# Kernel tuning notes

Hardware: AMD Instinct MI355X
Metric: run time of the kernel (lower is better)

The kernel has to match this reference:

```python
import jax, jax.numpy as jnp
import numpy as np

TEMP = 0.07  # softmax temperature T


def _l2norm(x, axis=1, eps=1e-12):
    return x / jnp.clip(jnp.linalg.norm(x, axis=axis, keepdims=True), eps, None)


def setup_inputs() -> dict:
    key = jax.random.key(0)
    k1, k2, k3, k4 = jax.random.split(key, 4)
    B, K, D = 256, 8192, 128
    q = jax.random.normal(k1, (B, D), dtype=jnp.float32)
    ba_queue = _l2norm(jax.random.normal(k2, (K, D), dtype=jnp.float32))
    nonba_queue = _l2norm(jax.random.normal(k3, (K, D), dtype=jnp.float32))
    targets = jax.random.randint(k4, (B,), 0, 2, dtype=jnp.int64)
    return {"q": q, "ba_queue": ba_queue, "nonba_queue": nonba_queue, "targets": targets}


def reference(q, ba_queue, nonba_queue, targets):
    K = ba_queue.shape[0]
    # encoder output is L2-normalized; queues are detached buffers
    qn = _l2norm(q, axis=1)
    all_feature = jnp.concatenate([qn, ba_queue, nonba_queue], axis=0)  # [N, D]
    all_label = jnp.concatenate([
        targets.astype(jnp.int32),
        jnp.ones((K,), dtype=jnp.int32),
        jnp.zeros((K,), dtype=jnp.int32),
    ])  # [N]
    N = all_feature.shape[0]

    # [N, N] similarity logits
    sim = jnp.matmul(all_feature, all_feature.T) / TEMP
    logits = sim - jax.lax.stop_gradient(jnp.max(sim, axis=1, keepdims=True))

    # positive mask (same label), excluding self
    mask = (all_label[:, None] == all_label[None, :]).astype(jnp.float32)
    logits_mask = 1.0 - jnp.eye(N, dtype=jnp.float32)
    mask = mask * logits_mask

    exp_logits = jnp.exp(logits) * logits_mask
    log_prob = logits - jnp.log(jnp.sum(exp_logits, axis=1, keepdims=True))
    mean_log_prob_pos = jnp.sum(mask * log_prob, axis=1) / jnp.sum(mask, axis=1)
    return -jnp.mean(mean_log_prob_pos)
```

## Files before the change

### kernel.cpp

```cpp
#include <hip/hip_runtime.h>
#include <hip/hip_bf16.h>
#include <stdint.h>

#define TEMPERATURE 0.07f
#define SC 20.6099312f

constexpr int NQ = 256;
constexpr int KQ = 8192;
constexpr int D  = 128;
constexpr int N  = NQ + 2 * KQ;
constexpr int CS = 26;
constexpr int BN = 128;
constexpr int RBM = N / 128;
constexpr int RBF = N / 256;

typedef float f32x16 __attribute__((ext_vector_type(16)));
typedef int   i32x4  __attribute__((ext_vector_type(4)));
typedef int   i32x8  __attribute__((ext_vector_type(8)));

constexpr size_t OFF_F32  = 0;
constexpr size_t OFF_8    = OFF_F32  + (size_t)NQ * D * 4;
constexpr size_t OFF_8S   = OFF_8    + (size_t)N * D;
constexpr size_t OFF_PART = OFF_8S   + (size_t)N * D;
constexpr size_t OFF_LP   = OFF_PART + (size_t)CS * N * 4;
constexpr size_t OFF_BSUM = OFF_LP   + (size_t)260 * 2 * 128 * 4;

#define MFMA8(a, b, c) __builtin_amdgcn_mfma_scale_f32_32x32x64_f8f6f4( \
    (a), (b), (c), 0, 0, 0, 0x7f7f7f7f, 0, 0x7f7f7f7f)

__global__ __launch_bounds__(256) void k_prep(const float* __restrict__ q,
                                              const float* __restrict__ ba,
                                              const float* __restrict__ nb,
                                              const long long* __restrict__ tgt,
                                              float* __restrict__ ff,
                                              unsigned char* __restrict__ fb8,
                                              unsigned char* __restrict__ fb8s,
                                              float* __restrict__ lp) {
    __shared__ float red[4][2][128];
    int wid = threadIdx.x >> 6, lane = threadIdx.x & 63;
    int rbase = blockIdx.x * 64 + wid * 16;
    float s0x = 0.f, s0y = 0.f, s1x = 0.f, s1y = 0.f;
    for (int i = 0; i < 16; ++i) {
        int r = rbase + i;
        const float* src = (r < NQ) ? (q + (size_t)r * D)
                         : (r < NQ + KQ) ? (ba + (size_t)(r - NQ) * D)
                         : (nb + (size_t)(r - NQ - KQ) * D);
        float2 v = *(const float2*)(src + lane * 2);
        float a = v.x, b = v.y;
        int lab;
        if (r < NQ) {
            float ss = a * a + b * b;
            #pragma unroll
            for (int m = 1; m < 64; m <<= 1) ss += __shfl_xor(ss, m);
            float scale = 1.0f / fmaxf(sqrtf(ss), 1e-12f);
            a *= scale; b *= scale;
            lab = (int)tgt[r];
            *(float2*)(ff + (size_t)r * D + lane * 2) = make_float2(a, b);
        } else {
            lab = (r < NQ + KQ) ? 1 : 0;
        }
        int w8  = __builtin_amdgcn_cvt_pk_fp8_f32(a, b, 0, false);
        int w8s = __builtin_amdgcn_cvt_pk_fp8_f32(a * SC, b * SC, 0, false);
        *(unsigned short*)(fb8  + (size_t)r * D + lane * 2) = (unsigned short)w8;
        *(unsigned short*)(fb8s + (size_t)r * D + lane * 2) = (unsigned short)w8s;
        if (lab) { s1x += a; s1y += b; } else { s0x += a; s0y += b; }
    }
    red[wid][0][lane * 2]     = s0x;
    red[wid][0][lane * 2 + 1] = s0y;
    red[wid][1][lane * 2]     = s1x;
    red[wid][1][lane * 2 + 1] = s1y;
    __syncthreads();
    int lab2 = threadIdx.x >> 7, d = threadIdx.x & 127;
    float s = red[0][lab2][d] + red[1][lab2][d] + red[2][lab2][d] + red[3][lab2][d];
    lp[((size_t)blockIdx.x * 2 + lab2) * 128 + d] = s;
}

__device__ __forceinline__ i32x8 lda(const unsigned char* buf, int wc, int l31,
                                     int lhi, int s, int cc) {
    int crow = wc * 64 + cc * 32 + l31;
    int line = crow >> 1;
    int pb = ((crow & 1) << 3) + s * 4 + lhi * 2;
    const unsigned char* lb = buf + line * 256;
    i32x4 lo = *(const i32x4*)(lb + ((pb    ) ^ (line & 15)) * 16);
    i32x4 hi = *(const i32x4*)(lb + ((pb + 1) ^ (line & 15)) * 16);
    i32x8 a = {lo[0], lo[1], lo[2], lo[3], hi[0], hi[1], hi[2], hi[3]};
    return a;
}

#define FIN(c) if (dofin) { const f32x16& A = pacc[((c) >> 2) & 1][((c) >> 1) & 1]; \
    float s_ = 0.f; \
    _Pragma("unroll") \
    for (int e = 0; e < 8; ++e) s_ += __builtin_amdgcn_exp2f(A[(((c) & 1) << 3) + e]); \
    ps[((c) >> 1) & 1] += s_; }

__device__ __forceinline__ void phase(const unsigned char* buf,
                                      f32x16 (&acc)[2][2], const f32x16 (&pacc)[2][2],
                                      const i32x8 (&rf)[2][2], const f32x16& z16,
                                      int wc, int l31, int lhi, bool dofin,
                                      float (&rsum)[2]) {
    i32x8 a00 = lda(buf, wc, l31, lhi, 0, 0);
    i32x8 a10 = lda(buf, wc, l31, lhi, 1, 0);
    i32x8 a01 = lda(buf, wc, l31, lhi, 0, 1);
    i32x8 a11 = lda(buf, wc, l31, lhi, 1, 1);
    float ps[2] = {0.f, 0.f};
    acc[0][0] = MFMA8(a00, rf[0][0], z16);       FIN(0)
    acc[0][0] = MFMA8(a10, rf[0][1], acc[0][0]); FIN(1)
    acc[0][1] = MFMA8(a00, rf[1][0], z16);       FIN(2)
    acc[0][1] = MFMA8(a10, rf[1][1], acc[0][1]); FIN(3)
    acc[1][0] = MFMA8(a01, rf[0][0], z16);       FIN(4)
    acc[1][0] = MFMA8(a11, rf[0][1], acc[1][0]); FIN(5)
    acc[1][1] = MFMA8(a01, rf[1][0], z16);       FIN(6)
    acc[1][1] = MFMA8(a11, rf[1][1], acc[1][1]); FIN(7)
    if (dofin) { rsum[0] += ps[0]; rsum[1] += ps[1]; }
}

__device__ __forceinline__ void fin_all(const f32x16 (&pacc)[2][2], float (&rsum)[2]) {
    #pragma unroll
    for (int cc = 0; cc < 2; ++cc)
        #pragma unroll
        for (int rs = 0; rs < 2; ++rs) {
            float p = 0.f;
            #pragma unroll
            for (int g = 0; g < 16; ++g)
                p += __builtin_amdgcn_exp2f(pacc[cc][rs][g]);
            rsum[rs] += p;
        }
}

__global__ __launch_bounds__(256, 2) void k_main(const unsigned char* __restrict__ fb8,
                                                 const unsigned char* __restrict__ fb8s,
                                                 float* __restrict__ part) {
    __shared__ __align__(16) unsigned char lds[2][BN * 128];
    const int bid = blockIdx.x;
    const int rb = bid / CS, cs = bid % CS;
    const int tid = threadIdx.x;
    const int lane = tid & 63;
    const int wid  = tid >> 6;
    const int wr = wid >> 1, wc = wid & 1;
    const int l31 = lane & 31, lhi = lane >> 5;
    const int rw = rb * 128 + wr * 64;

    int soff[4];
    #pragma unroll
    for (int i = 0; i < 4; ++i) {
        int flat = i * 256 + tid;
        int line = flat >> 4, p = flat & 15;
        int pl = p ^ (line & 15);
        soff[i] = (2 * line + (pl >> 3)) * 128 + (pl & 7) * 16;
    }

#define STAGE(T, B) { \
    const unsigned char* base_ = fb8 + ((size_t)(cs + (T) * CS)) * (BN * 128); \
    _Pragma("unroll") \
    for (int i_ = 0; i_ < 4; ++i_) \
        __builtin_amdgcn_global_load_lds( \
            (const __attribute__((address_space(1))) unsigned int*)(base_ + soff[i_]), \
            (__attribute__((address_space(3))) unsigned int*)(&lds[B][(i_ * 256 + tid) * 16]), \
            16, 0, 0); }

#define SYNC() { asm volatile("s_waitcnt vmcnt(0)" ::: "memory"); __builtin_amdgcn_s_barrier(); }

    i32x8 rf[2][2];
    #pragma unroll
    for (int rs = 0; rs < 2; ++rs)
        #pragma unroll
        for (int s = 0; s < 2; ++s)
            rf[rs][s] = *(const i32x8*)(fb8s + (size_t)(rw + rs * 32 + l31) * D + s * 64 + lhi * 32);

    f32x16 z16;
    #pragma unroll
    for (int e = 0; e < 16; ++e) z16[e] = 0.f;

    float rsum[2] = {0.f, 0.f};
    f32x16 accA[2][2], accB[2][2];

    STAGE(0, 0) SYNC()
    STAGE(1, 1)
    phase(lds[0], accA, accB, rf, z16, wc, l31, lhi, false, rsum);
    SYNC()
    STAGE(2, 0)
    phase(lds[1], accB, accA, rf, z16, wc, l31, lhi, true, rsum);
    SYNC()
    STAGE(3, 1)
    phase(lds[0], accA, accB, rf, z16, wc, l31, lhi, true, rsum);
    SYNC()
    STAGE(4, 0)
    phase(lds[1], accB, accA, rf, z16, wc, l31, lhi, true, rsum);
    SYNC()
    phase(lds[0], accA, accB, rf, z16, wc, l31, lhi, true, rsum);
    fin_all(accA, rsum);

    rsum[0] += __shfl_xor(rsum[0], 32);
    rsum[1] += __shfl_xor(rsum[1], 32);
    __shared__ float xred[2][2][32];
    if (wc == 0 && lane < 32) {
        xred[wr][0][lane] = rsum[0];
        xred[wr][1][lane] = rsum[1];
    }
    __syncthreads();
    if (wc == 1 && lane < 32) {
        part[(size_t)cs * N + rw + lane]      = xred[wr][0][lane] + rsum[0];
        part[(size_t)cs * N + rw + 32 + lane] = xred[wr][1][lane] + rsum[1];
    }
#undef STAGE
#undef SYNC
}

__global__ __launch_bounds__(256) void k_rowfin(const float* __restrict__ part,
                                                const float* __restrict__ ff,
                                                const float* __restrict__ ba,
                                                const float* __restrict__ nb,
                                                const float* __restrict__ lp,
                                                const long long* __restrict__ tgt,
                                                float* __restrict__ bsum) {
    __shared__ float sS[256];
    __shared__ float red[256];
    __shared__ int scnt[2];
    {
        int lab = threadIdx.x >> 7, d = threadIdx.x & 127;
        float s[4] = {0.f, 0.f, 0.f, 0.f};
        for (int b = 0; b < 260; b += 4) {
            #pragma unroll
            for (int j = 0; j < 4; ++j)
                s[j] += lp[((size_t)(b + j) * 2 + lab) * 128 + d];
        }
        sS[threadIdx.x] = (s[0] + s[1]) + (s[2] + s[3]);
        if (threadIdx.x < 64) {
            int c = 0;
            #pragma unroll
            for (int i = 0; i < 4; ++i) c += (int)tgt[threadIdx.x + 64 * i];
            #pragma unroll
            for (int m = 1; m < 64; m <<= 1) c += __shfl_xor(c, m);
            if (threadIdx.x == 0) { scnt[0] = (NQ - c) + KQ; scnt[1] = c + KQ; }
        }
    }
    __syncthreads();
    int r = blockIdx.x * 256 + threadIdx.x;
    float se = 0.f;
    #pragma unroll
    for (int c = 0; c < CS; ++c) se += part[(size_t)c * N + r];
    int lab = (r < NQ) ? (int)tgt[r] : ((r < NQ + KQ) ? 1 : 0);
    const float* fsrc = (r < NQ) ? (ff + (size_t)r * D)
                      : (r < NQ + KQ) ? (ba + (size_t)(r - NQ) * D)
                      : (nb + (size_t)(r - NQ - KQ) * D);
    const float4* frow = (const float4*)fsrc;
    const float4* srow = (const float4*)(sS + lab * 128);
    float dS = 0.f, dd = 0.f;
    #pragma unroll
    for (int i = 0; i < 32; ++i) {
        float4 f = frow[i];
        float4 s = srow[i];
        dS += f.x * s.x + f.y * s.y + f.z * s.z + f.w * s.w;
        int wa  = __builtin_amdgcn_cvt_pk_fp8_f32(f.x, f.y, 0, false);
        int wb  = __builtin_amdgcn_cvt_pk_fp8_f32(f.z, f.w, 0, false);
        int wsa = __builtin_amdgcn_cvt_pk_fp8_f32(f.x * SC, f.y * SC, 0, false);
        int wsb = __builtin_amdgcn_cvt_pk_fp8_f32(f.z * SC, f.w * SC, 0, false);
        dd += __builtin_amdgcn_cvt_f32_fp8(wa, 0) * __builtin_amdgcn_cvt_f32_fp8(wsa, 0)
            + __builtin_amdgcn_cvt_f32_fp8(wa, 1) * __builtin_amdgcn_cvt_f32_fp8(wsa, 1)
            + __builtin_amdgcn_cvt_f32_fp8(wb, 0) * __builtin_amdgcn_cvt_f32_fp8(wsb, 0)
            + __builtin_amdgcn_cvt_f32_fp8(wb, 1) * __builtin_amdgcn_cvt_f32_fp8(wsb, 1);
    }
    se -= __builtin_amdgcn_exp2f(dd);
    float lse = logf(se);
    float P = (float)(scnt[lab] - 1);
    float mlpp = (dS - 1.0f) / (TEMPERATURE * P) - lse;
    red[threadIdx.x] = mlpp;
    __syncthreads();
    for (int s2 = 128; s2 > 0; s2 >>= 1) {
        if (threadIdx.x < s2) red[threadIdx.x] += red[threadIdx.x + s2];
        __syncthreads();
    }
    if (threadIdx.x == 0) bsum[blockIdx.x] = red[0];
}

__global__ __launch_bounds__(64) void k_final(const float* __restrict__ bsum,
                                              float* __restrict__ out) {
    float s = bsum[threadIdx.x];
    if (threadIdx.x == 0) s += bsum[64];
    #pragma unroll
    for (int m = 1; m < 64; m <<= 1) s += __shfl_xor(s, m);
    if (threadIdx.x == 0) out[0] = -s / (float)N;
}

extern "C" void kernel_launch(void* const* d_in, const int* in_sizes, int n_in,
                              void* d_out, int out_size, void* d_ws, size_t ws_size,
                              hipStream_t stream) {
    const float* q       = (const float*)d_in[0];
    const float* ba      = (const float*)d_in[1];
    const float* nb      = (const float*)d_in[2];
    const long long* tgt = (const long long*)d_in[3];
    char* ws = (char*)d_ws;
    float*         ff   = (float*)(ws + OFF_F32);
    unsigned char* fb8  = (unsigned char*)(ws + OFF_8);
    unsigned char* fb8s = (unsigned char*)(ws + OFF_8S);
    float*         part = (float*)(ws + OFF_PART);
    float*         lp   = (float*)(ws + OFF_LP);
    float*         bsum = (float*)(ws + OFF_BSUM);

    k_prep  <<<260,      256, 0, stream>>>(q, ba, nb, tgt, ff, fb8, fb8s, lp);
    k_main  <<<RBM * CS, 256, 0, stream>>>(fb8, fb8s, part);
    k_rowfin<<<RBF,      256, 0, stream>>>(part, ff, ba, nb, lp, tgt, bsum);
    k_final <<<1,         64, 0, stream>>>(bsum, (float*)d_out);
}
```

Measured before the change: 79.68 us.

## Load column tiles directly from global memory instead of LDS double-buffering

Removes the LDS staging buffers, async global-to-LDS loads and barriers in the main similarity kernel. Each wave now loads its FP8 column fragments straight into registers from global memory and runs the MFMA and exp2 accumulation in a simple loop. Occupancy hint goes from 2 to 3 blocks per CU. This drops LDS traffic and barrier synchronisation, but gives up the software pipelining that overlapped loads with the previous tile's exp work, and each tile's data is now fetched from global/L2 by both wave rows instead of once per block.

```diff
diff --git a/kernel.cpp b/kernel.cpp
--- a/kernel.cpp
+++ b/kernel.cpp
@@ -15,7 +15,6 @@
 constexpr int RBF = N / 256;
 
 typedef float f32x16 __attribute__((ext_vector_type(16)));
-typedef int   i32x4  __attribute__((ext_vector_type(4)));
 typedef int   i32x8  __attribute__((ext_vector_type(8)));
 
 constexpr size_t OFF_F32  = 0;
@@ -75,62 +74,9 @@
     lp[((size_t)blockIdx.x * 2 + lab2) * 128 + d] = s;
 }
 
-__device__ __forceinline__ i32x8 lda(const unsigned char* buf, int wc, int l31,
-                                     int lhi, int s, int cc) {
-    int crow = wc * 64 + cc * 32 + l31;
-    int line = crow >> 1;
-    int pb = ((crow & 1) << 3) + s * 4 + lhi * 2;
-    const unsigned char* lb = buf + line * 256;
-    i32x4 lo = *(const i32x4*)(lb + ((pb    ) ^ (line & 15)) * 16);
-    i32x4 hi = *(const i32x4*)(lb + ((pb + 1) ^ (line & 15)) * 16);
-    i32x8 a = {lo[0], lo[1], lo[2], lo[3], hi[0], hi[1], hi[2], hi[3]};
-    return a;
-}
-
-#define FIN(c) if (dofin) { const f32x16& A = pacc[((c) >> 2) & 1][((c) >> 1) & 1]; \
-    float s_ = 0.f; \
-    _Pragma("unroll") \
-    for (int e = 0; e < 8; ++e) s_ += __builtin_amdgcn_exp2f(A[(((c) & 1) << 3) + e]); \
-    ps[((c) >> 1) & 1] += s_; }
-
-__device__ __forceinline__ void phase(const unsigned char* buf,
-                                      f32x16 (&acc)[2][2], const f32x16 (&pacc)[2][2],
-                                      const i32x8 (&rf)[2][2], const f32x16& z16,
-                                      int wc, int l31, int lhi, bool dofin,
-                                      float (&rsum)[2]) {
-    i32x8 a00 = lda(buf, wc, l31, lhi, 0, 0);
-    i32x8 a10 = lda(buf, wc, l31, lhi, 1, 0);
-    i32x8 a01 = lda(buf, wc, l31, lhi, 0, 1);
-    i32x8 a11 = lda(buf, wc, l31, lhi, 1, 1);
-    float ps[2] = {0.f, 0.f};
-    acc[0][0] = MFMA8(a00, rf[0][0], z16);       FIN(0)
-    acc[0][0] = MFMA8(a10, rf[0][1], acc[0][0]); FIN(1)
-    acc[0][1] = MFMA8(a00, rf[1][0], z16);       FIN(2)
-    acc[0][1] = MFMA8(a10, rf[1][1], acc[0][1]); FIN(3)
-    acc[1][0] = MFMA8(a01, rf[0][0], z16);       FIN(4)
-    acc[1][0] = MFMA8(a11, rf[0][1], acc[1][0]); FIN(5)
-    acc[1][1] = MFMA8(a01, rf[1][0], z16);       FIN(6)
-    acc[1][1] = MFMA8(a11, rf[1][1], acc[1][1]); FIN(7)
-    if (dofin) { rsum[0] += ps[0]; rsum[1] += ps[1]; }
-}
-
-__device__ __forceinline__ void fin_all(const f32x16 (&pacc)[2][2], float (&rsum)[2]) {
-    #pragma unroll
-    for (int cc = 0; cc < 2; ++cc)
-        #pragma unroll
-        for (int rs = 0; rs < 2; ++rs) {
-            float p = 0.f;
-            #pragma unroll
-            for (int g = 0; g < 16; ++g)
-                p += __builtin_amdgcn_exp2f(pacc[cc][rs][g]);
-            rsum[rs] += p;
-        }
-}
-
-__global__ __launch_bounds__(256, 2) void k_main(const unsigned char* __restrict__ fb8,
+__global__ __launch_bounds__(256, 3) void k_main(const unsigned char* __restrict__ fb8,
                                                  const unsigned char* __restrict__ fb8s,
                                                  float* __restrict__ part) {
-    __shared__ __align__(16) unsigned char lds[2][BN * 128];
     const int bid = blockIdx.x;
     const int rb = bid / CS, cs = bid % CS;
     const int tid = threadIdx.x;
@@ -140,26 +86,6 @@
     const int l31 = lane & 31, lhi = lane >> 5;
     const int rw = rb * 128 + wr * 64;
 
-    int soff[4];
-    #pragma unroll
-    for (int i = 0; i < 4; ++i) {
-        int flat = i * 256 + tid;
-        int line = flat >> 4, p = flat & 15;
-        int pl = p ^ (line & 15);
-        soff[i] = (2 * line + (pl >> 3)) * 128 + (pl & 7) * 16;
-    }
-
-#define STAGE(T, B) { \
-    const unsigned char* base_ = fb8 + ((size_t)(cs + (T) * CS)) * (BN * 128); \
-    _Pragma("unroll") \
-    for (int i_ = 0; i_ < 4; ++i_) \
-        __builtin_amdgcn_global_load_lds( \
-            (const __attribute__((address_space(1))) unsigned int*)(base_ + soff[i_]), \
-            (__attribute__((address_space(3))) unsigned int*)(&lds[B][(i_ * 256 + tid) * 16]), \
-            16, 0, 0); }
-
-#define SYNC() { asm volatile("s_waitcnt vmcnt(0)" ::: "memory"); __builtin_amdgcn_s_barrier(); }
-
     i32x8 rf[2][2];
     #pragma unroll
     for (int rs = 0; rs < 2; ++rs)
@@ -167,28 +93,46 @@
         for (int s = 0; s < 2; ++s)
             rf[rs][s] = *(const i32x8*)(fb8s + (size_t)(rw + rs * 32 + l31) * D + s * 64 + lhi * 32);
 
+    const unsigned char* abase = fb8 + ((size_t)(wc * 64 + l31)) * D + lhi * 32;
+
     f32x16 z16;
     #pragma unroll
     for (int e = 0; e < 16; ++e) z16[e] = 0.f;
 
-    float rsum[2] = {0.f, 0.f};
-    f32x16 accA[2][2], accB[2][2];
-
-    STAGE(0, 0) SYNC()
-    STAGE(1, 1)
-    phase(lds[0], accA, accB, rf, z16, wc, l31, lhi, false, rsum);
-    SYNC()
-    STAGE(2, 0)
-    phase(lds[1], accB, accA, rf, z16, wc, l31, lhi, true, rsum);
-    SYNC()
-    STAGE(3, 1)
-    phase(lds[0], accA, accB, rf, z16, wc, l31, lhi, true, rsum);
-    SYNC()
-    STAGE(4, 0)
-    phase(lds[1], accB, accA, rf, z16, wc, l31, lhi, true, rsum);
-    SYNC()
-    phase(lds[0], accA, accB, rf, z16, wc, l31, lhi, true, rsum);
-    fin_all(accA, rsum);
+    float2 ps2[2] = {{0.f, 0.f}, {0.f, 0.f}};
+    f32x16 acc[2][2];
+
+    for (int t = 0; t < 5; ++t) {
+        const unsigned char* tb = abase + (size_t)(cs + t * CS) * 128 * D;
+        i32x8 a_c0s0 = *(const i32x8*)(tb);
+        i32x8 a_c0s1 = *(const i32x8*)(tb + 64);
+        i32x8 a_c1s0 = *(const i32x8*)(tb + 32 * D);
+        i32x8 a_c1s1 = *(const i32x8*)(tb + 32 * D + 64);
+
+        acc[0][0] = MFMA8(a_c0s0, rf[0][0], z16);
+        acc[0][0] = MFMA8(a_c0s1, rf[0][1], acc[0][0]);
+        acc[0][1] = MFMA8(a_c0s0, rf[1][0], z16);
+        acc[0][1] = MFMA8(a_c0s1, rf[1][1], acc[0][1]);
+        acc[1][0] = MFMA8(a_c1s0, rf[0][0], z16);
+        acc[1][0] = MFMA8(a_c1s1, rf[0][1], acc[1][0]);
+        acc[1][1] = MFMA8(a_c1s0, rf[1][0], z16);
+        acc[1][1] = MFMA8(a_c1s1, rf[1][1], acc[1][1]);
+
+        #pragma unroll
+        for (int cc = 0; cc < 2; ++cc)
+            #pragma unroll
+            for (int rs = 0; rs < 2; ++rs) {
+                float2 p = {0.f, 0.f};
+                #pragma unroll
+                for (int g = 0; g < 8; ++g) {
+                    p.x += __builtin_amdgcn_exp2f(acc[cc][rs][2 * g]);
+                    p.y += __builtin_amdgcn_exp2f(acc[cc][rs][2 * g + 1]);
+                }
+                ps2[rs].x += p.x; ps2[rs].y += p.y;
+            }
+    }
+
+    float rsum[2] = {ps2[0].x + ps2[0].y, ps2[1].x + ps2[1].y};
 
     rsum[0] += __shfl_xor(rsum[0], 32);
     rsum[1] += __shfl_xor(rsum[1], 32);
@@ -202,8 +146,6 @@
         part[(size_t)cs * N + rw + lane]      = xred[wr][0][lane] + rsum[0];
         part[(size_t)cs * N + rw + 32 + lane] = xred[wr][1][lane] + rsum[1];
     }
-#undef STAGE
-#undef SYNC
 }
 
 __global__ __launch_bounds__(256) void k_rowfin(const float* __restrict__ part,
```

Measured after the change: 111.0 us. 39.3% more time.
